# Performance work log

Measured on AMD Instinct MI355X. Metric: run time of the kernel, lower is better.

Reference implementation:

```python
import jax, jax.numpy as jnp
import numpy as np

FILL = -100  # SentimentClasses.FILLUP_POLARITY_VALUE, also CrossEntropyLoss ignore_index
B, T, S, C = 512, 8, 8192, 3


def setup_inputs() -> dict:
    key = jax.random.key(0)
    k1, k2, k3 = jax.random.split(key, 3)
    predictions = jax.random.normal(k1, (B, C, S), dtype=jnp.float32)
    true_classes = jax.random.randint(k2, (B, T), 0, 3, dtype=jnp.int64)
    raw = jax.random.randint(k3, (B, T, S), 0, 2, dtype=jnp.int64)
    # keep at most one target per (batch, seq) position so the original's
    # conflict check would never fire (mask rows are disjoint)
    cum = jnp.cumsum(raw, axis=1)
    true_target_mask = ((raw == 1) & (cum == 1)).astype(jnp.int64)
    return {"predictions": predictions, "true_classes": true_classes,
            "true_target_mask": true_target_mask}


def reference(predictions, true_classes, true_target_mask):
    # Vectorized replacement of the nested scatter loop:
    # position (b,s) gets class of the (unique) target whose mask is 1, else FILL.
    valid_t = (true_classes != FILL)[:, :, None] & (true_target_mask == 1)  # [B,T,S]
    true_sequence = jnp.max(
        jnp.where(valid_t, true_classes[:, :, None], FILL), axis=1)  # [B,S]

    # CrossEntropyLoss(ignore_index=FILL) over class axis (axis=1)
    logp = jax.nn.log_softmax(predictions, axis=1)  # [B,C,S]
    valid = true_sequence != FILL  # [B,S]
    tgt_safe = jnp.where(valid, true_sequence, 0)
    nll = -jnp.take_along_axis(logp, tgt_safe[:, None, :], axis=1)[:, 0, :]  # [B,S]
    n_valid = jnp.maximum(jnp.sum(valid), 1).astype(nll.dtype)
    return jnp.sum(jnp.where(valid, nll, 0.0)) / n_valid
```

## Files before the change

kernel.cpp:

```cpp
#include <hip/hip_runtime.h>

namespace {

constexpr int FILL = -100;
constexpr int B = 512, T = 8, S = 8192, C = 3;
constexpr int THREADS = 256;
constexpr int SB = S / 4;
constexpr int BLOCKS = 2048;

typedef int   iv4 __attribute__((ext_vector_type(4)));
typedef float fv4 __attribute__((ext_vector_type(4)));

__global__ __launch_bounds__(THREADS) void seq_loss_partial(
    const fv4* __restrict__ predv,
    const int* __restrict__ cls,
    const iv4* __restrict__ maskv,
    float* __restrict__ part_sum,
    int*   __restrict__ part_cnt)
{
    const int b0 = blockIdx.x >> 3;
    const int b1 = b0 + 256;
    const int s4 = ((blockIdx.x & 7) << 8) + threadIdx.x;

    iv4 m0[T], m1[T];
    #pragma unroll
    for (int t = 0; t < T; ++t)
        m0[t] = __builtin_nontemporal_load(&maskv[(b0 * T + t) * SB + s4]);
    #pragma unroll
    for (int t = 0; t < T; ++t)
        m1[t] = __builtin_nontemporal_load(&maskv[(b1 * T + t) * SB + s4]);

    const fv4 a0 = __builtin_nontemporal_load(&predv[(b0 * C + 0) * SB + s4]);
    const fv4 a1 = __builtin_nontemporal_load(&predv[(b0 * C + 1) * SB + s4]);
    const fv4 a2 = __builtin_nontemporal_load(&predv[(b0 * C + 2) * SB + s4]);
    const fv4 d0 = __builtin_nontemporal_load(&predv[(b1 * C + 0) * SB + s4]);
    const fv4 d1 = __builtin_nontemporal_load(&predv[(b1 * C + 1) * SB + s4]);
    const fv4 d2 = __builtin_nontemporal_load(&predv[(b1 * C + 2) * SB + s4]);

    int ce0[T], ce1[T];
    #pragma unroll
    for (int t = 0; t < T; ++t) {
        const int c0 = cls[b0 * T + t];
        const int c1 = cls[b1 * T + t];
        ce0[t] = (c0 != FILL) ? (c0 + 1) : 0;
        ce1[t] = (c1 != FILL) ? (c1 + 1) : 0;
    }

    float lsum = 0.0f;
    int   lcnt = 0;

    auto consume = [&](const iv4* m, const int* ce,
                       const fv4& p0, const fv4& p1, const fv4& p2) {
        int sx = 0, sy = 0, sz = 0, sw = 0;
        #pragma unroll
        for (int t = 0; t < T; ++t) {
            sx += m[t].x * ce[t];
            sy += m[t].y * ce[t];
            sz += m[t].z * ce[t];
            sw += m[t].w * ce[t];
        }
        auto acc = [&](int sum, float x0, float x1, float x2) {
            if (sum > 0) {
                const float lse = __logf(__expf(x0) + __expf(x1) + __expf(x2));
                const float xt  = (sum == 1) ? x0 : ((sum == 2) ? x1 : x2);
                lsum += lse - xt;
                ++lcnt;
            }
        };
        acc(sx, p0.x, p1.x, p2.x);
        acc(sy, p0.y, p1.y, p2.y);
        acc(sz, p0.z, p1.z, p2.z);
        acc(sw, p0.w, p1.w, p2.w);
    };
    consume(m0, ce0, a0, a1, a2);
    consume(m1, ce1, d0, d1, d2);

    #pragma unroll
    for (int off = 32; off > 0; off >>= 1) {
        lsum += __shfl_down(lsum, off);
        lcnt += __shfl_down(lcnt, off);
    }
    __shared__ float sm_s[THREADS / 64];
    __shared__ int   sm_c[THREADS / 64];
    const int lane = threadIdx.x & 63, wv = threadIdx.x >> 6;
    if (lane == 0) { sm_s[wv] = lsum; sm_c[wv] = lcnt; }
    __syncthreads();
    if (threadIdx.x == 0) {
        float s = 0.0f; int cc = 0;
        #pragma unroll
        for (int i = 0; i < THREADS / 64; ++i) { s += sm_s[i]; cc += sm_c[i]; }
        part_sum[blockIdx.x] = s;
        part_cnt[blockIdx.x] = cc;
    }
}

__global__ __launch_bounds__(256) void seq_loss_final(
    const float* __restrict__ part_sum,
    const int*   __restrict__ part_cnt,
    float*       __restrict__ out)
{
    double s = 0.0, c = 0.0;
    for (int i = threadIdx.x; i < BLOCKS; i += 256) {
        s += (double)part_sum[i];
        c += (double)part_cnt[i];
    }
    #pragma unroll
    for (int off = 32; off > 0; off >>= 1) {
        s += __shfl_down(s, off);
        c += __shfl_down(c, off);
    }
    __shared__ double ds[4], dc[4];
    const int lane = threadIdx.x & 63, wv = threadIdx.x >> 6;
    if (lane == 0) { ds[wv] = s; dc[wv] = c; }
    __syncthreads();
    if (threadIdx.x == 0) {
        double st = ds[0] + ds[1] + ds[2] + ds[3];
        double ct = dc[0] + dc[1] + dc[2] + dc[3];
        if (ct < 1.0) ct = 1.0;
        out[0] = (float)(st / ct);
    }
}

}

extern "C" void kernel_launch(void* const* d_in, const int* in_sizes, int n_in,
                              void* d_out, int out_size, void* d_ws, size_t ws_size,
                              hipStream_t stream) {
    const fv4* predv = (const fv4*)d_in[0];
    const int* cls   = (const int*)d_in[1];
    const iv4* maskv = (const iv4*)d_in[2];

    float* part_sum = (float*)d_ws;
    int*   part_cnt = (int*)((char*)d_ws + BLOCKS * sizeof(float));
    float* out      = (float*)d_out;

    seq_loss_partial<<<BLOCKS, THREADS, 0, stream>>>(predv, cls, maskv,
                                                     part_sum, part_cnt);
    seq_loss_final<<<1, 256, 0, stream>>>(part_sum, part_cnt, out);
}
```

Measured before the change: 208.5 us.

## Assign one batch row per block with software-pipelined tile loop

```diff
diff --git a/kernel.cpp b/kernel.cpp
--- a/kernel.cpp
+++ b/kernel.cpp
@@ -6,60 +6,52 @@
 constexpr int B = 512, T = 8, S = 8192, C = 3;
 constexpr int THREADS = 256;
 constexpr int SB = S / 4;
-constexpr int BLOCKS = 2048;
+constexpr int TILES = SB / THREADS;
+constexpr int BLOCKS_P = B;
 
 typedef int   iv4 __attribute__((ext_vector_type(4)));
 typedef float fv4 __attribute__((ext_vector_type(4)));
 
-__global__ __launch_bounds__(THREADS) void seq_loss_partial(
+__global__ __launch_bounds__(THREADS, 2) void seq_loss_partial(
     const fv4* __restrict__ predv,
     const int* __restrict__ cls,
     const iv4* __restrict__ maskv,
     float* __restrict__ part_sum,
     int*   __restrict__ part_cnt)
 {
-    const int b0 = blockIdx.x >> 3;
-    const int b1 = b0 + 256;
-    const int s4 = ((blockIdx.x & 7) << 8) + threadIdx.x;
+    const int b = blockIdx.x;
+    const iv4* mrow = maskv + (size_t)b * T * SB;
+    const fv4* prow = predv + (size_t)b * C * SB;
 
-    iv4 m0[T], m1[T];
-    #pragma unroll
-    for (int t = 0; t < T; ++t)
-        m0[t] = __builtin_nontemporal_load(&maskv[(b0 * T + t) * SB + s4]);
-    #pragma unroll
-    for (int t = 0; t < T; ++t)
-        m1[t] = __builtin_nontemporal_load(&maskv[(b1 * T + t) * SB + s4]);
-
-    const fv4 a0 = __builtin_nontemporal_load(&predv[(b0 * C + 0) * SB + s4]);
-    const fv4 a1 = __builtin_nontemporal_load(&predv[(b0 * C + 1) * SB + s4]);
-    const fv4 a2 = __builtin_nontemporal_load(&predv[(b0 * C + 2) * SB + s4]);
-    const fv4 d0 = __builtin_nontemporal_load(&predv[(b1 * C + 0) * SB + s4]);
-    const fv4 d1 = __builtin_nontemporal_load(&predv[(b1 * C + 1) * SB + s4]);
-    const fv4 d2 = __builtin_nontemporal_load(&predv[(b1 * C + 2) * SB + s4]);
-
-    int ce0[T], ce1[T];
+    unsigned ce[T];
     #pragma unroll
     for (int t = 0; t < T; ++t) {
-        const int c0 = cls[b0 * T + t];
-        const int c1 = cls[b1 * T + t];
-        ce0[t] = (c0 != FILL) ? (c0 + 1) : 0;
-        ce1[t] = (c1 != FILL) ? (c1 + 1) : 0;
+        const int c = cls[b * T + t];
+        ce[t] = (c != FILL) ? (unsigned)(c + 1) & 7u : 0u;
     }
 
     float lsum = 0.0f;
     int   lcnt = 0;
 
-    auto consume = [&](const iv4* m, const int* ce,
-                       const fv4& p0, const fv4& p1, const fv4& p2) {
-        int sx = 0, sy = 0, sz = 0, sw = 0;
+    auto load_tile = [&](int s4, iv4* m, fv4& p0, fv4& p1, fv4& p2) {
+        #pragma unroll
+        for (int t = 0; t < T; ++t)
+            m[t] = __builtin_nontemporal_load(&mrow[t * SB + s4]);
+        p0 = __builtin_nontemporal_load(&prow[0 * SB + s4]);
+        p1 = __builtin_nontemporal_load(&prow[1 * SB + s4]);
+        p2 = __builtin_nontemporal_load(&prow[2 * SB + s4]);
+    };
+
+    auto consume = [&](const iv4* m, const fv4& p0, const fv4& p1, const fv4& p2) {
+        unsigned sx = 0, sy = 0, sz = 0, sw = 0;
         #pragma unroll
         for (int t = 0; t < T; ++t) {
-            sx += m[t].x * ce[t];
-            sy += m[t].y * ce[t];
-            sz += m[t].z * ce[t];
-            sw += m[t].w * ce[t];
+            sx += ((unsigned)m[t].x & 1u) * ce[t];
+            sy += ((unsigned)m[t].y & 1u) * ce[t];
+            sz += ((unsigned)m[t].z & 1u) * ce[t];
+            sw += ((unsigned)m[t].w & 1u) * ce[t];
         }
-        auto acc = [&](int sum, float x0, float x1, float x2) {
+        auto acc = [&](unsigned sum, float x0, float x1, float x2) {
             if (sum > 0) {
                 const float lse = __logf(__expf(x0) + __expf(x1) + __expf(x2));
                 const float xt  = (sum == 1) ? x0 : ((sum == 2) ? x1 : x2);
@@ -72,8 +64,21 @@
         acc(sz, p0.z, p1.z, p2.z);
         acc(sw, p0.w, p1.w, p2.w);
     };
-    consume(m0, ce0, a0, a1, a2);
-    consume(m1, ce1, d0, d1, d2);
+
+    iv4 mc[T]; fv4 c0, c1, c2;
+    load_tile(threadIdx.x, mc, c0, c1, c2);
+    #pragma unroll
+    for (int i = 0; i < TILES; ++i) {
+        iv4 mn[T]; fv4 n0, n1, n2;
+        if (i + 1 < TILES)
+            load_tile(threadIdx.x + (i + 1) * THREADS, mn, n0, n1, n2);
+        consume(mc, c0, c1, c2);
+        if (i + 1 < TILES) {
+            #pragma unroll
+            for (int t = 0; t < T; ++t) mc[t] = mn[t];
+            c0 = n0; c1 = n1; c2 = n2;
+        }
+    }
 
     #pragma unroll
     for (int off = 32; off > 0; off >>= 1) {
@@ -100,7 +105,7 @@
     float*       __restrict__ out)
 {
     double s = 0.0, c = 0.0;
-    for (int i = threadIdx.x; i < BLOCKS; i += 256) {
+    for (int i = threadIdx.x; i < BLOCKS_P; i += 256) {
         s += (double)part_sum[i];
         c += (double)part_cnt[i];
     }
@@ -131,10 +136,10 @@
     const iv4* maskv = (const iv4*)d_in[2];
 
     float* part_sum = (float*)d_ws;
-    int*   part_cnt = (int*)((char*)d_ws + BLOCKS * sizeof(float));
+    int*   part_cnt = (int*)((char*)d_ws + BLOCKS_P * sizeof(float));
     float* out      = (float*)d_out;
 
-    seq_loss_partial<<<BLOCKS, THREADS, 0, stream>>>(predv, cls, maskv,
-                                                     part_sum, part_cnt);
+    seq_loss_partial<<<BLOCKS_P, THREADS, 0, stream>>>(predv, cls, maskv,
+                                                       part_sum, part_cnt);
     seq_loss_final<<<1, 256, 0, stream>>>(part_sum, part_cnt, out);
 }
```

Result: slower. 215.3 us (+3.2%).
